# Kernel tuning notes

Hardware: AMD Instinct MI355X
Metric: run time of the kernel (lower is better)

The kernel has to match this reference:

```python
import jax, jax.numpy as jnp
import numpy as np

B, C, PC, P = 64, 32, 128, 2048
N = B * C * PC          # 262144 graph nodes
E = 2097152             # ~8 edges per node


def _gcn(x, src, dst, n, W, b):
    # PyG GCNConv: add self loops, sym-normalized mean aggregation of x@W
    xw = x @ W
    sl = jnp.arange(n, dtype=src.dtype)
    s = jnp.concatenate([src, sl]); d = jnp.concatenate([dst, sl])
    deg = jax.ops.segment_sum(jnp.ones(d.shape, xw.dtype), d, num_segments=n)
    dinv = jax.lax.rsqrt(deg)  # deg >= 1 thanks to self loops
    norm = dinv[s] * dinv[d]
    return jax.ops.segment_sum(xw[s] * norm[:, None], d, num_segments=n) + b


def _gat(x, src, dst, n, W, a_src, a_dst, b):
    # PyG GATConv (heads=1): self loops, edge softmax over incoming edges
    xw = x @ W
    sl = jnp.arange(n, dtype=src.dtype)
    s = jnp.concatenate([src, sl]); d = jnp.concatenate([dst, sl])
    e = jax.nn.leaky_relu((xw @ a_src)[s] + (xw @ a_dst)[d], 0.2)
    m = jax.ops.segment_max(jax.lax.stop_gradient(e), d, num_segments=n)
    ex = jnp.exp(e - m[d])
    denom = jax.ops.segment_sum(ex, d, num_segments=n)
    alpha = ex / denom[d]
    return jax.ops.segment_sum(xw[s] * alpha[:, None], d, num_segments=n) + b


def _cross_edges(num_cross, batch_size):
    # faithful to get_c_adjacency: every ordered pair (i!=j) appears twice per graph
    ii, jj = np.meshgrid(np.arange(num_cross), np.arange(num_cross), indexing='ij')
    m = ii != jj
    s, d = ii[m], jj[m]
    s2 = np.concatenate([s, d]); d2 = np.concatenate([d, s])
    off = (np.arange(batch_size) * num_cross)[:, None]
    src = (s2[None] + off).reshape(-1)
    dst = (d2[None] + off).reshape(-1)
    return jnp.asarray(src, jnp.int32), jnp.asarray(dst, jnp.int32)


def _conv1d(x, W, b):
    y = jax.lax.conv_general_dilated(x, W, (2,), ((1, 1),), dimension_numbers=('NCH', 'OIH', 'NCH'))
    return y + b[None, :, None]


def _bn_eval(x, gamma, beta):
    # BatchNorm1d in eval mode with default running stats (mean 0, var 1)
    scale = gamma / np.float32(np.sqrt(1.0 + 1e-5))
    return x * scale[None, :, None] + beta[None, :, None]


def setup_inputs() -> dict:
    key = jax.random.key(0)
    ks = jax.random.split(key, 32)
    rn = lambda k, sh, s=0.1: (jax.random.normal(k, sh, jnp.float32) * s)
    return {
        'x': jax.random.normal(ks[0], (N, 19), jnp.float32),
        'edge_index': jax.random.randint(ks[1], (2, E), 0, N, jnp.int32),
        'points': jax.random.normal(ks[2], (B, 3, P), jnp.float32),
        'W1': rn(ks[3], (19, 32)), 'b1': rn(ks[4], (32,)),
        'W2': rn(ks[5], (32, 64)), 'b2': rn(ks[6], (64,)),
        'W3': rn(ks[7], (64, 64)), 'b3': rn(ks[8], (64,)),
        'Wg1': rn(ks[9], (64, 64)), 'asrc1': rn(ks[10], (64,)), 'adst1': rn(ks[11], (64,)), 'bg1': rn(ks[12], (64,)),
        'Wg2': rn(ks[13], (64, 64)), 'asrc2': rn(ks[14], (64,)), 'adst2': rn(ks[15], (64,)), 'bg2': rn(ks[16], (64,)),
        'c1W': rn(ks[17], (32, 3, 3)), 'c1b': rn(ks[18], (32,)),
        'g1': 1.0 + rn(ks[19], (32,)), 'be1': rn(ks[20], (32,)),
        'c2W': rn(ks[21], (64, 32, 3)), 'c2b': rn(ks[22], (64,)),
        'g2': 1.0 + rn(ks[23], (64,)), 'be2': rn(ks[24], (64,)),
        'c3W': rn(ks[25], (64, 64, 3)), 'c3b': rn(ks[26], (64,)),
        'Wl2': rn(ks[27], (64, 64)), 'bl2': rn(ks[28], (64,)),
        'Wl3': rn(ks[29], (64, 1)), 'bl3': rn(ks[30], (1,)),
        'batch_size': B, 'num_cross': C, 'num_pieces': PC,
    }


def reference(x, edge_index, points, W1, b1, W2, b2, W3, b3,
              Wg1, asrc1, adst1, bg1, Wg2, asrc2, adst2, bg2,
              c1W, c1b, g1, be1, c2W, c2b, g2, be2, c3W, c3b,
              Wl2, bl2, Wl3, bl3, batch_size, num_cross, num_pieces):
    src, dst = edge_index[0], edge_index[1]
    n = x.shape[0]
    h = jax.nn.relu(_gcn(x, src, dst, n, W1, b1))  # dropout is a no-op in eval
    h = jax.nn.leaky_relu(_gcn(h, src, dst, n, W2, b2), 0.01)
    h = jax.nn.leaky_relu(_gcn(h, src, dst, n, W3, b3), 0.01)
    h = _gat(h, src, dst, n, Wg1, asrc1, adst1, bg1)
    h = h.reshape(batch_size, num_cross, num_pieces, -1).mean(-2)  # [B, C, 64]
    s2, d2 = _cross_edges(num_cross, batch_size)
    h = _gat(h.reshape(batch_size * num_cross, 64), s2, d2, batch_size * num_cross, Wg2, asrc2, adst2, bg2)
    h = h.reshape(batch_size, num_cross, 64).mean(1)  # [B, 64]
    p = _bn_eval(jax.nn.leaky_relu(_conv1d(points, c1W, c1b), 0.01), g1, be1)
    p = _bn_eval(jax.nn.leaky_relu(_conv1d(p, c2W, c2b), 0.01), g2, be2)
    p = jax.nn.leaky_relu(_conv1d(p, c3W, c3b), 0.01).mean(-1)  # AdaptiveAvgPool1d(1).squeeze -> [B, 64]
    h = h + p
    h = jax.nn.leaky_relu(h @ Wl2 + bl2, 0.01)
    return jax.nn.sigmoid(h @ Wl3 + bl3)  # [B, 1]
```

## Files before the change

kernel.cpp:

```cpp
#include <hip/hip_runtime.h>
#include <cstdint>
#include <cstddef>

#define NN 262144
#define EE 2097152
#define BB 64
#define CCROSS 32
#define PCC 128
#define PP 2048
#define NBUCK 256
#define BCAP 12288

typedef _Float16 f16;
typedef __attribute__((ext_vector_type(4))) _Float16 f16x4;
typedef __attribute__((ext_vector_type(8))) _Float16 f16x8;
typedef __attribute__((ext_vector_type(4))) float f32x4;

static __device__ __forceinline__ float lrelu(float x, float s) { return x > 0.f ? x : s * x; }

__global__ __launch_bounds__(256) void bucket_a_k(const int* __restrict__ src, const int* __restrict__ dst,
                                                  unsigned* __restrict__ buckets, int* __restrict__ gcnt) {
    __shared__ int hist[NBUCK];
    __shared__ int base[NBUCK];
    __shared__ unsigned short rankbuf[8192];
    const int tid = threadIdx.x;
    const int e0 = blockIdx.x * 8192;
    hist[tid] = 0;
    __syncthreads();
    for (int i = tid; i < 8192; i += 256) {
        int d = dst[e0 + i];
        rankbuf[i] = (unsigned short)atomicAdd(&hist[d >> 10], 1);
    }
    __syncthreads();
    base[tid] = tid * BCAP + atomicAdd(&gcnt[tid], hist[tid]);
    __syncthreads();
    for (int i = tid; i < 8192; i += 256) {
        int s = src[e0 + i];
        int d = dst[e0 + i];
        int b = d >> 10;
        buckets[base[b] + rankbuf[i]] = ((unsigned)s << 10) | (unsigned)(d & 1023);
    }
}

__global__ void bucket_scan_k(const int* __restrict__ gcnt, int* __restrict__ bbase, int* __restrict__ rp) {
    __shared__ int tmp[256];
    int tid = threadIdx.x;
    int v = gcnt[tid];
    tmp[tid] = v;
    __syncthreads();
    for (int off = 1; off < 256; off <<= 1) {
        int t = (tid >= off) ? tmp[tid - off] : 0;
        __syncthreads();
        tmp[tid] += t;
        __syncthreads();
    }
    bbase[tid] = tmp[tid] - v;
    if (tid == 0) rp[NN] = EE;
}

__global__ __launch_bounds__(256) void bucket_b_k(const unsigned* __restrict__ buckets, const int* __restrict__ gcnt,
                                                  const int* __restrict__ bbase, int* __restrict__ rp,
                                                  float* __restrict__ dinv, int* __restrict__ col) {
    __shared__ int cnt[1024];
    __shared__ int scan[1024];
    __shared__ int wsum[256];
    const int b = blockIdx.x;
    const int tid = threadIdx.x;
    int n = gcnt[b];
    if (n > BCAP) n = BCAP;
    const unsigned* eb = buckets + (size_t)b * BCAP;
    const int gb = bbase[b];
    for (int i = tid; i < 1024; i += 256) cnt[i] = 0;
    __syncthreads();
    for (int i = tid; i < n; i += 256) atomicAdd(&cnt[eb[i] & 1023], 1);
    __syncthreads();
    int b4 = tid * 4;
    int c0 = cnt[b4], c1 = cnt[b4 + 1], c2 = cnt[b4 + 2], c3 = cnt[b4 + 3];
    int tsum = c0 + c1 + c2 + c3;
    wsum[tid] = tsum;
    __syncthreads();
    for (int off = 1; off < 256; off <<= 1) {
        int t = (tid >= off) ? wsum[tid - off] : 0;
        __syncthreads();
        wsum[tid] += t;
        __syncthreads();
    }
    int excl = wsum[tid] - tsum;
    scan[b4] = excl;
    scan[b4 + 1] = excl + c0;
    scan[b4 + 2] = excl + c0 + c1;
    scan[b4 + 3] = excl + c0 + c1 + c2;
    int vbase = b * 1024 + b4;
    rp[vbase + 0] = gb + scan[b4 + 0];
    rp[vbase + 1] = gb + scan[b4 + 1];
    rp[vbase + 2] = gb + scan[b4 + 2];
    rp[vbase + 3] = gb + scan[b4 + 3];
    dinv[vbase + 0] = rsqrtf((float)(c0 + 1));
    dinv[vbase + 1] = rsqrtf((float)(c1 + 1));
    dinv[vbase + 2] = rsqrtf((float)(c2 + 1));
    dinv[vbase + 3] = rsqrtf((float)(c3 + 1));
    __syncthreads();
    for (int i = tid; i < 1024; i += 256) cnt[i] = 0;
    __syncthreads();
    for (int i = tid; i < n; i += 256) {
        unsigned p = eb[i];
        int dl = p & 1023;
        int r = atomicAdd(&cnt[dl], 1);
        col[gb + scan[dl] + r] = (int)(p >> 10);
    }
}

__global__ void zprep_k(const float* __restrict__ x, const float* __restrict__ dinv, f16* __restrict__ z) {
    int v = blockIdx.x * 256 + threadIdx.x;
    if (v >= NN) return;
    float dv = dinv[v];
    const float* xr = x + (size_t)v * 19;
    float vv[20];
#pragma unroll
    for (int k = 0; k < 19; k++) vv[k] = dv * xr[k];
    vv[19] = 0.f;
    f16x4* zr = (f16x4*)(z + (size_t)v * 32);
#pragma unroll
    for (int c = 0; c < 5; c++) {
        f16x4 t = {(f16)vv[4 * c], (f16)vv[4 * c + 1], (f16)vv[4 * c + 2], (f16)vv[4 * c + 3]};
        zr[c] = t;
    }
    f16x4 zz = {(f16)0.f, (f16)0.f, (f16)0.f, (f16)0.f};
#pragma unroll
    for (int c = 5; c < 8; c++) zr[c] = zz;
}

#define ZSTR1 36
template <int KINR, int KOUT, int ACT>
__global__ __launch_bounds__(256) void fused_agg_gemm_k(const f16* __restrict__ z, const int* __restrict__ rp,
                                                        const int* __restrict__ col, const float* __restrict__ Wg,
                                                        const float* __restrict__ dinv, const float* __restrict__ bias,
                                                        f16* __restrict__ zout) {
    constexpr int NO = KOUT / 4;
    __shared__ float Wl[32 * KOUT];
    __shared__ float zrow[64 * ZSTR1];
    const int tid = threadIdx.x;
    for (int i = tid; i < 32 * KOUT; i += 256) Wl[i] = (i < KINR * KOUT) ? Wg[i] : 0.f;

    const int r = tid >> 2;
    const int idx = tid & 3;
    const int v = blockIdx.x * 64 + r;
    const f16x8* z8 = (const f16x8*)z;
    f16x8 a = z8[(size_t)v * 4 + idx];
    float acc8[8];
#pragma unroll
    for (int j = 0; j < 8; j++) acc8[j] = (float)a[j];
    int st = rp[v], e = rp[v + 1];
    int i = st;
    for (; i + 4 <= e; i += 4) {
        int u0 = col[i], u1 = col[i + 1], u2 = col[i + 2], u3 = col[i + 3];
        f16x8 a0 = z8[(size_t)u0 * 4 + idx];
        f16x8 a1 = z8[(size_t)u1 * 4 + idx];
        f16x8 a2 = z8[(size_t)u2 * 4 + idx];
        f16x8 a3 = z8[(size_t)u3 * 4 + idx];
#pragma unroll
        for (int j = 0; j < 8; j++)
            acc8[j] += ((float)a0[j] + (float)a1[j]) + ((float)a2[j] + (float)a3[j]);
    }
    for (; i < e; i++) {
        f16x8 aa = z8[(size_t)col[i] * 4 + idx];
#pragma unroll
        for (int j = 0; j < 8; j++) acc8[j] += (float)aa[j];
    }
    float4 s0, s1;
    s0.x = acc8[0]; s0.y = acc8[1]; s0.z = acc8[2]; s0.w = acc8[3];
    s1.x = acc8[4]; s1.y = acc8[5]; s1.z = acc8[6]; s1.w = acc8[7];
    *(float4*)&zrow[r * ZSTR1 + idx * 8] = s0;
    *(float4*)&zrow[r * ZSTR1 + idx * 8 + 4] = s1;
    __syncthreads();

    float acc[NO];
#pragma unroll
    for (int j = 0; j < NO; j++) acc[j] = 0.f;
#pragma unroll 4
    for (int k = 0; k < 32; k++) {
        float zv = zrow[r * ZSTR1 + k];
        const float* wr = Wl + k * KOUT + NO * idx;
#pragma unroll
        for (int j = 0; j < NO; j++) acc[j] = fmaf(zv, wr[j], acc[j]);
    }
    float dv = dinv[v];
    f16 hv[NO];
#pragma unroll
    for (int j = 0; j < NO; j++) {
        float o = dv * acc[j] + bias[NO * idx + j];
        o = (ACT == 0) ? fmaxf(o, 0.f) : lrelu(o, 0.01f);
        hv[j] = (f16)(o * dv);
    }
    if constexpr (NO == 8) {
        f16x8 h = {hv[0], hv[1], hv[2], hv[3], hv[4], hv[5], hv[6], hv[7]};
        *(f16x8*)(zout + (size_t)v * KOUT + NO * idx) = h;
    } else {
        f16x8 h0 = {hv[0], hv[1], hv[2], hv[3], hv[4], hv[5], hv[6], hv[7]};
        f16x8 h1 = {hv[8], hv[9], hv[10], hv[11], hv[12], hv[13], hv[14], hv[15]};
        f16x8* yo = (f16x8*)(zout + (size_t)v * KOUT + NO * idx);
        yo[0] = h0; yo[1] = h1;
    }
}

__global__ __launch_bounds__(256) void agg_h16_k(const f16* __restrict__ y, const int* __restrict__ rp,
                                                 const int* __restrict__ col, f16* __restrict__ out) {
    int gid = blockIdx.x * 256 + threadIdx.x;
    int v = gid >> 3;
    int idx = gid & 7;
    const f16x8* y8 = (const f16x8*)y;
    f16x8 a = y8[(size_t)v * 8 + idx];
    float acc[8];
#pragma unroll
    for (int j = 0; j < 8; j++) acc[j] = (float)a[j];
    int s = rp[v], e = rp[v + 1];
    int i = s;
    for (; i + 4 <= e; i += 4) {
        int u0 = col[i], u1 = col[i + 1], u2 = col[i + 2], u3 = col[i + 3];
        f16x8 a0 = y8[(size_t)u0 * 8 + idx];
        f16x8 a1 = y8[(size_t)u1 * 8 + idx];
        f16x8 a2 = y8[(size_t)u2 * 8 + idx];
        f16x8 a3 = y8[(size_t)u3 * 8 + idx];
#pragma unroll
        for (int j = 0; j < 8; j++)
            acc[j] += ((float)a0[j] + (float)a1[j]) + ((float)a2[j] + (float)a3[j]);
    }
    for (; i < e; i++) {
        f16x8 aa = y8[(size_t)col[i] * 8 + idx];
#pragma unroll
        for (int j = 0; j < 8; j++) acc[j] += (float)aa[j];
    }
    f16x8 r;
#pragma unroll
    for (int j = 0; j < 8; j++) r[j] = (f16)acc[j];
    ((f16x8*)out)[(size_t)v * 8 + idx] = r;
}

__global__ void pack_w_k(const float* __restrict__ W, f16* __restrict__ out) {
    int o = blockIdx.x * 256 + threadIdx.x;
    if (o >= 4096) return;
    int frag = o >> 9;
    int kt = frag >> 2;
    int c = frag & 3;
    int idx = o & 511;
    int l = idx >> 3;
    int j = idx & 7;
    int k = kt * 32 + ((l >> 4) << 3) + j;
    int n = 16 * c + (l & 15);
    out[o] = (f16)W[k * 64 + n];
}

#define HSTR 72
__global__ __launch_bounds__(256) void gemm3_gat_k(const f16* __restrict__ aggz, const f16* __restrict__ w3p,
                                                   const float* __restrict__ dinv, const float* __restrict__ b3,
                                                   const f16* __restrict__ wgp, const float* __restrict__ av,
                                                   const float* __restrict__ ad, f16* __restrict__ xw,
                                                   float* __restrict__ es, float* __restrict__ ed) {
    __shared__ f16 zin[64 * HSTR];
    __shared__ f16 hh[64 * HSTR];
    const int tid = threadIdx.x;
    const int v0 = blockIdx.x * 64;
    {
        int row = tid >> 2;
        int kb = (tid & 3) * 16;
        const f16x8* zp = (const f16x8*)(aggz + (size_t)(v0 + row) * 64 + kb);
        f16x8 z0 = zp[0], z1 = zp[1];
        *(f16x8*)&zin[row * HSTR + kb] = z0;
        *(f16x8*)&zin[row * HSTR + kb + 8] = z1;
    }
    __syncthreads();

    const int w = tid >> 6;
    const int l = tid & 63;
    const int m = l & 15;
    const int q = l >> 4;
    const int r0 = 16 * w;

    f32x4 acc0 = {0.f, 0.f, 0.f, 0.f}, acc1 = acc0, acc2 = acc0, acc3 = acc0;
#pragma unroll
    for (int kt = 0; kt < 2; kt++) {
        f16x8 afrag = *(const f16x8*)&zin[(r0 + m) * HSTR + kt * 32 + q * 8];
        f16x8 b0 = *(const f16x8*)&w3p[((kt * 4 + 0) << 9) + l * 8];
        f16x8 b1 = *(const f16x8*)&w3p[((kt * 4 + 1) << 9) + l * 8];
        f16x8 b2 = *(const f16x8*)&w3p[((kt * 4 + 2) << 9) + l * 8];
        f16x8 b3f = *(const f16x8*)&w3p[((kt * 4 + 3) << 9) + l * 8];
        acc0 = __builtin_amdgcn_mfma_f32_16x16x32_f16(afrag, b0, acc0, 0, 0, 0);
        acc1 = __builtin_amdgcn_mfma_f32_16x16x32_f16(afrag, b1, acc1, 0, 0, 0);
        acc2 = __builtin_amdgcn_mfma_f32_16x16x32_f16(afrag, b2, acc2, 0, 0, 0);
        acc3 = __builtin_amdgcn_mfma_f32_16x16x32_f16(afrag, b3f, acc3, 0, 0, 0);
    }
    {
        float dv0 = dinv[v0 + r0 + q * 4 + 0];
        float dv1 = dinv[v0 + r0 + q * 4 + 1];
        float dv2 = dinv[v0 + r0 + q * 4 + 2];
        float dv3 = dinv[v0 + r0 + q * 4 + 3];
#pragma unroll
        for (int c = 0; c < 4; c++) {
            const f32x4* ac = (c == 0) ? &acc0 : (c == 1) ? &acc1 : (c == 2) ? &acc2 : &acc3;
            float bb = b3[16 * c + m];
            hh[(r0 + q * 4 + 0) * HSTR + 16 * c + m] = (f16)lrelu(dv0 * (*ac)[0] + bb, 0.01f);
            hh[(r0 + q * 4 + 1) * HSTR + 16 * c + m] = (f16)lrelu(dv1 * (*ac)[1] + bb, 0.01f);
            hh[(r0 + q * 4 + 2) * HSTR + 16 * c + m] = (f16)lrelu(dv2 * (*ac)[2] + bb, 0.01f);
            hh[(r0 + q * 4 + 3) * HSTR + 16 * c + m] = (f16)lrelu(dv3 * (*ac)[3] + bb, 0.01f);
        }
    }
    __syncthreads();

    acc0 = (f32x4){0.f, 0.f, 0.f, 0.f}; acc1 = acc0; acc2 = acc0; acc3 = acc0;
#pragma unroll
    for (int kt = 0; kt < 2; kt++) {
        f16x8 afrag = *(const f16x8*)&hh[(r0 + m) * HSTR + kt * 32 + q * 8];
        f16x8 b0 = *(const f16x8*)&wgp[((kt * 4 + 0) << 9) + l * 8];
        f16x8 b1 = *(const f16x8*)&wgp[((kt * 4 + 1) << 9) + l * 8];
        f16x8 b2 = *(const f16x8*)&wgp[((kt * 4 + 2) << 9) + l * 8];
        f16x8 b3f = *(const f16x8*)&wgp[((kt * 4 + 3) << 9) + l * 8];
        acc0 = __builtin_amdgcn_mfma_f32_16x16x32_f16(afrag, b0, acc0, 0, 0, 0);
        acc1 = __builtin_amdgcn_mfma_f32_16x16x32_f16(afrag, b1, acc1, 0, 0, 0);
        acc2 = __builtin_amdgcn_mfma_f32_16x16x32_f16(afrag, b2, acc2, 0, 0, 0);
        acc3 = __builtin_amdgcn_mfma_f32_16x16x32_f16(afrag, b3f, acc3, 0, 0, 0);
    }
    {
        float e1[4] = {0.f, 0.f, 0.f, 0.f}, e2[4] = {0.f, 0.f, 0.f, 0.f};
#pragma unroll
        for (int c = 0; c < 4; c++) {
            const f32x4* ac = (c == 0) ? &acc0 : (c == 1) ? &acc1 : (c == 2) ? &acc2 : &acc3;
            float a1 = av[16 * c + m];
            float d1 = ad[16 * c + m];
#pragma unroll
            for (int reg = 0; reg < 4; reg++) {
                float g = (*ac)[reg];
                e1[reg] = fmaf(g, a1, e1[reg]);
                e2[reg] = fmaf(g, d1, e2[reg]);
                xw[(size_t)(v0 + r0 + q * 4 + reg) * 64 + 16 * c + m] = (f16)g;
            }
        }
#pragma unroll
        for (int reg = 0; reg < 4; reg++) {
            e1[reg] += __shfl_xor(e1[reg], 1); e1[reg] += __shfl_xor(e1[reg], 2);
            e1[reg] += __shfl_xor(e1[reg], 4); e1[reg] += __shfl_xor(e1[reg], 8);
            e2[reg] += __shfl_xor(e2[reg], 1); e2[reg] += __shfl_xor(e2[reg], 2);
            e2[reg] += __shfl_xor(e2[reg], 4); e2[reg] += __shfl_xor(e2[reg], 8);
        }
        if (m == 0) {
#pragma unroll
            for (int reg = 0; reg < 4; reg++) {
                es[v0 + r0 + q * 4 + reg] = e1[reg];
                ed[v0 + r0 + q * 4 + reg] = e2[reg];
            }
        }
    }
}

__global__ void gat_w_k(const float* __restrict__ es, const float* __restrict__ ed,
                        const int* __restrict__ rp, const int* __restrict__ col,
                        f16* __restrict__ ew, float* __restrict__ wself, float* __restrict__ invden) {
    int v = blockIdx.x * 256 + threadIdx.x;
    if (v >= NN) return;
    float edv = ed[v];
    float eself = lrelu(es[v] + edv, 0.2f);
    float m = eself;
    int s = rp[v], e = rp[v + 1];
    int i = s;
    float lg[32];
    for (; i + 4 <= e; i += 4) {
        int u0 = col[i], u1 = col[i + 1], u2 = col[i + 2], u3 = col[i + 3];
        float t0 = lrelu(es[u0] + edv, 0.2f);
        float t1 = lrelu(es[u1] + edv, 0.2f);
        float t2 = lrelu(es[u2] + edv, 0.2f);
        float t3 = lrelu(es[u3] + edv, 0.2f);
        int k = i - s;
        if (k + 3 < 32) { lg[k] = t0; lg[k + 1] = t1; lg[k + 2] = t2; lg[k + 3] = t3; }
        m = fmaxf(m, fmaxf(fmaxf(t0, t1), fmaxf(t2, t3)));
    }
    for (; i < e; i++) {
        float t = lrelu(es[col[i]] + edv, 0.2f);
        int k = i - s;
        if (k < 32) lg[k] = t;
        m = fmaxf(m, t);
    }
    float wsl = __expf(eself - m);
    float den = wsl;
    for (i = s; i < e; i++) {
        int k = i - s;
        float t = (k < 32) ? lg[k] : lrelu(es[col[i]] + edv, 0.2f);
        float w = __expf(t - m);
        ew[i] = (f16)w;
        den += w;
    }
    wself[v] = wsl;
    invden[v] = 1.f / den;
}

__global__ __launch_bounds__(256) void gat_agg_h_k(const f16* __restrict__ y, const int* __restrict__ rp,
                                                   const int* __restrict__ col, const f16* __restrict__ ew,
                                                   const float* __restrict__ wself, const float* __restrict__ invden,
                                                   const float* __restrict__ bias, float* __restrict__ out) {
    int gid = blockIdx.x * 256 + threadIdx.x;
    int v = gid >> 3;
    int idx = gid & 7;
    const f16x8* y8 = (const f16x8*)y;
    float ws = wself[v];
    f16x8 self = y8[(size_t)v * 8 + idx];
    float acc[8];
#pragma unroll
    for (int j = 0; j < 8; j++) acc[j] = ws * (float)self[j];
    int s = rp[v], e = rp[v + 1];
    int i = s;
    for (; i + 4 <= e; i += 4) {
        int u0 = col[i], u1 = col[i + 1], u2 = col[i + 2], u3 = col[i + 3];
        float w0 = (float)ew[i], w1 = (float)ew[i + 1], w2 = (float)ew[i + 2], w3 = (float)ew[i + 3];
        f16x8 a0 = y8[(size_t)u0 * 8 + idx];
        f16x8 a1 = y8[(size_t)u1 * 8 + idx];
        f16x8 a2 = y8[(size_t)u2 * 8 + idx];
        f16x8 a3 = y8[(size_t)u3 * 8 + idx];
#pragma unroll
        for (int j = 0; j < 8; j++)
            acc[j] = fmaf(w0, (float)a0[j], fmaf(w1, (float)a1[j], fmaf(w2, (float)a2[j], fmaf(w3, (float)a3[j], acc[j]))));
    }
    for (; i < e; i++) {
        float w = (float)ew[i];
        f16x8 aa = y8[(size_t)col[i] * 8 + idx];
#pragma unroll
        for (int j = 0; j < 8; j++) acc[j] = fmaf(w, (float)aa[j], acc[j]);
    }
    float inv = invden[v];
    const float4* b4 = (const float4*)(bias + 8 * idx);
    float4 bb0 = b4[0], bb1 = b4[1];
    float4 o0, o1;
    o0.x = acc[0] * inv + bb0.x; o0.y = acc[1] * inv + bb0.y;
    o0.z = acc[2] * inv + bb0.z; o0.w = acc[3] * inv + bb0.w;
    o1.x = acc[4] * inv + bb1.x; o1.y = acc[5] * inv + bb1.y;
    o1.z = acc[6] * inv + bb1.z; o1.w = acc[7] * inv + bb1.w;
    float4* op = (float4*)(out + (size_t)v * 64 + 8 * idx);
    op[0] = o0; op[1] = o1;
}

__global__ void pool_pieces_k(const float* __restrict__ in, float* __restrict__ out) {
    int gid = blockIdx.x * 256 + threadIdx.x;
    if (gid >= BB * CCROSS * 64) return;
    int f = gid & 63, g = gid >> 6;
    const float* p = in + (size_t)g * PCC * 64 + f;
    float s = 0.f;
#pragma unroll 8
    for (int i = 0; i < PCC; i++) s += p[(size_t)i * 64];
    out[gid] = s * (1.f / 128.f);
}

__global__ void pool_cross_k(const float* __restrict__ in, float* __restrict__ out) {
    int gid = blockIdx.x * 64 + threadIdx.x;
    if (gid >= BB * 64) return;
    int f = gid & 63, b = gid >> 6;
    const float* p = in + (size_t)b * CCROSS * 64 + f;
    float s = 0.f;
#pragma unroll
    for (int i = 0; i < CCROSS; i++) s += p[(size_t)i * 64];
    out[gid] = s * (1.f / 32.f);
}

template <int KIN, int KOUT>
__global__ void gat_gemm_k(const float* __restrict__ x, const float* __restrict__ W,
                           float* __restrict__ y, const float* __restrict__ av, const float* __restrict__ ad,
                           float* __restrict__ es, float* __restrict__ ed, int n) {
    int v = blockIdx.x * 256 + threadIdx.x;
    if (v >= n) return;
    const float* xr = x + (size_t)v * KIN;
    float acc[KOUT];
#pragma unroll
    for (int j = 0; j < KOUT; j++) acc[j] = 0.f;
#pragma unroll 2
    for (int k = 0; k < KIN; k++) {
        float xv = xr[k];
#pragma unroll
        for (int j = 0; j < KOUT; j++) acc[j] = fmaf(xv, W[k * KOUT + j], acc[j]);
    }
    float e1 = 0.f, e2 = 0.f;
    float4* y4 = (float4*)(y + (size_t)v * KOUT);
#pragma unroll
    for (int j4 = 0; j4 < KOUT / 4; j4++) {
        float4 t;
        t.x = acc[4 * j4 + 0]; t.y = acc[4 * j4 + 1]; t.z = acc[4 * j4 + 2]; t.w = acc[4 * j4 + 3];
        y4[j4] = t;
        e1 = fmaf(t.x, av[4 * j4 + 0], e1); e1 = fmaf(t.y, av[4 * j4 + 1], e1);
        e1 = fmaf(t.z, av[4 * j4 + 2], e1); e1 = fmaf(t.w, av[4 * j4 + 3], e1);
        e2 = fmaf(t.x, ad[4 * j4 + 0], e2); e2 = fmaf(t.y, ad[4 * j4 + 1], e2);
        e2 = fmaf(t.z, ad[4 * j4 + 2], e2); e2 = fmaf(t.w, ad[4 * j4 + 3], e2);
    }
    es[v] = e1; ed[v] = e2;
}

__global__ void cross_att_k(const float* __restrict__ xw, const float* __restrict__ es,
                            const float* __restrict__ ed, const float* __restrict__ bg,
                            float* __restrict__ out) {
    int gid = blockIdx.x * 256 + threadIdx.x;
    if (gid >= BB * CCROSS * 64) return;
    int f = gid & 63;
    int d = (gid >> 6) & 31;
    int g = gid >> 11;
    int base = g * CCROSS;
    float edd = ed[base + d];
    float m = -1e30f;
#pragma unroll
    for (int s = 0; s < CCROSS; s++) {
        float e = lrelu(es[base + s] + edd, 0.2f);
        m = fmaxf(m, e);
    }
    float den = 0.f, acc = 0.f;
#pragma unroll
    for (int s = 0; s < CCROSS; s++) {
        float e = lrelu(es[base + s] + edd, 0.2f);
        float w = __expf(e - m) * ((s == d) ? 1.f : 2.f);
        den += w;
        acc = fmaf(w, xw[(size_t)(base + s) * 64 + f], acc);
    }
    out[gid] = acc / den + bg[f];
}

#define S0_STR 264
#define S1_STR 132
#define S2_STR 66
#define S0_OFF 0
#define S1_OFF (3 * S0_STR)
#define S2_OFF (S1_OFF + 32 * S1_STR)
#define SMEM_FLOATS (S2_OFF + 64 * S2_STR)

__global__ __launch_bounds__(256) void conv_fused_k(
        const float* __restrict__ pts, const float* __restrict__ c1W, const float* __restrict__ c1b,
        const float* __restrict__ g1, const float* __restrict__ be1,
        const float* __restrict__ c2W, const float* __restrict__ c2b,
        const float* __restrict__ g2, const float* __restrict__ be2,
        const float* __restrict__ c3W, const float* __restrict__ c3b,
        float* __restrict__ partials) {
    __shared__ float smem[SMEM_FLOATS];
    float* s0 = smem + S0_OFF;
    float* s1 = smem + S1_OFF;
    float* s2 = smem + S2_OFF;
    float* s3 = smem;

    const int b = blockIdx.x >> 3;
    const int q = blockIdx.x & 7;
    const int tid = threadIdx.x;
    const float bnscale = 0.99999500003749968f;

    const int lo0 = 256 * q - 7;
    for (int t = tid; t < 3 * 263; t += 256) {
        int c = t / 263, j = t - c * 263;
        int p = lo0 + j;
        s0[c * S0_STR + j] = (p >= 0 && p < PP) ? pts[((size_t)b * 3 + c) * PP + p] : 0.f;
    }
    __syncthreads();

    const int lo1 = 128 * q - 3;
    for (int t = tid; t < 32 * 131; t += 256) {
        int ch = t / 131, j = t - ch * 131;
        int p1 = lo1 + j;
        float v = 0.f;
        if (p1 >= 0 && p1 < 1024) {
            float acc = c1b[ch];
            const float* w = c1W + ch * 9;
            const float* x0 = s0 + 2 * j;
#pragma unroll
            for (int ci = 0; ci < 3; ci++) {
                acc = fmaf(x0[ci * S0_STR + 0], w[ci * 3 + 0], acc);
                acc = fmaf(x0[ci * S0_STR + 1], w[ci * 3 + 1], acc);
                acc = fmaf(x0[ci * S0_STR + 2], w[ci * 3 + 2], acc);
            }
            acc = lrelu(acc, 0.01f);
            v = fmaf(acc, g1[ch] * bnscale, be1[ch]);
        }
        s1[ch * S1_STR + j] = v;
    }
    __syncthreads();

    const int lo2 = 64 * q - 1;
    for (int t = tid; t < 64 * 65; t += 256) {
        int ch = t / 65, j = t - ch * 65;
        int p2 = lo2 + j;
        float v = 0.f;
        if (p2 >= 0 && p2 < 512) {
            float acc = c2b[ch];
            const float* w = c2W + ch * 96;
            const float* x1 = s1 + 2 * j;
#pragma unroll
            for (int ci = 0; ci < 32; ci++) {
                acc = fmaf(x1[ci * S1_STR + 0], w[ci * 3 + 0], acc);
                acc = fmaf(x1[ci * S1_STR + 1], w[ci * 3 + 1], acc);
                acc = fmaf(x1[ci * S1_STR + 2], w[ci * 3 + 2], acc);
            }
            acc = lrelu(acc, 0.01f);
            v = fmaf(acc, g2[ch] * bnscale, be2[ch]);
        }
        s2[ch * S2_STR + j] = v;
    }
    __syncthreads();

    for (int t = tid; t < 64 * 32; t += 256) {
        int o = t >> 5, j = t & 31;
        float acc = c3b[o];
        const float* w = c3W + o * 192;
        const float* x2 = s2 + 2 * j;
#pragma unroll 16
        for (int ci = 0; ci < 64; ci++) {
            acc = fmaf(x2[ci * S2_STR + 0], w[ci * 3 + 0], acc);
            acc = fmaf(x2[ci * S2_STR + 1], w[ci * 3 + 1], acc);
            acc = fmaf(x2[ci * S2_STR + 2], w[ci * 3 + 2], acc);
        }
        s3[t] = lrelu(acc, 0.01f);
    }
    __syncthreads();

    if (tid < 64) {
        float s = 0.f;
#pragma unroll
        for (int j = 0; j < 32; j++) s += s3[tid * 32 + j];
        partials[((size_t)b * 8 + q) * 64 + tid] = s;
    }
}

__global__ void head_k(const float* __restrict__ hG, const float* __restrict__ partials,
                       const float* __restrict__ Wl2, const float* __restrict__ bl2,
                       const float* __restrict__ Wl3, const float* __restrict__ bl3,
                       float* __restrict__ out) {
    int b = blockIdx.x;
    int f = threadIdx.x;
    __shared__ float sh[64];
    float p = 0.f;
#pragma unroll
    for (int q = 0; q < 8; q++) p += partials[((size_t)b * 8 + q) * 64 + f];
    float h = hG[b * 64 + f] + p * (1.f / 256.f);
    sh[f] = h;
    __syncthreads();
    float acc = bl2[f];
#pragma unroll
    for (int k = 0; k < 64; k++) acc = fmaf(sh[k], Wl2[k * 64 + f], acc);
    acc = lrelu(acc, 0.01f);
    float pr = acc * Wl3[f];
#pragma unroll
    for (int off = 32; off > 0; off >>= 1) pr += __shfl_down(pr, off, 64);
    if (f == 0) out[b] = 1.f / (1.f + __expf(-(pr + bl3[0])));
}

extern "C" void kernel_launch(void* const* d_in, const int* in_sizes, int n_in,
                              void* d_out, int out_size, void* d_ws, size_t ws_size,
                              hipStream_t stream) {
    const float* x = (const float*)d_in[0];
    const int* ei = (const int*)d_in[1];
    const float* points = (const float*)d_in[2];
    const float* W1 = (const float*)d_in[3];
    const float* b1 = (const float*)d_in[4];
    const float* W2 = (const float*)d_in[5];
    const float* b2 = (const float*)d_in[6];
    const float* W3 = (const float*)d_in[7];
    const float* b3 = (const float*)d_in[8];
    const float* Wg1 = (const float*)d_in[9];
    const float* asrc1 = (const float*)d_in[10];
    const float* adst1 = (const float*)d_in[11];
    const float* bg1 = (const float*)d_in[12];
    const float* Wg2 = (const float*)d_in[13];
    const float* asrc2 = (const float*)d_in[14];
    const float* adst2 = (const float*)d_in[15];
    const float* bg2 = (const float*)d_in[16];
    const float* c1W = (const float*)d_in[17];
    const float* c1b = (const float*)d_in[18];
    const float* g1 = (const float*)d_in[19];
    const float* be1 = (const float*)d_in[20];
    const float* c2W = (const float*)d_in[21];
    const float* c2b = (const float*)d_in[22];
    const float* g2 = (const float*)d_in[23];
    const float* be2 = (const float*)d_in[24];
    const float* c3W = (const float*)d_in[25];
    const float* c3b = (const float*)d_in[26];
    const float* Wl2 = (const float*)d_in[27];
    const float* bl2 = (const float*)d_in[28];
    const float* Wl3 = (const float*)d_in[29];
    const float* bl3 = (const float*)d_in[30];

    const int* src = ei;
    const int* dst = ei + EE;

    char* w = (char*)d_ws;
    size_t off = 0;
    auto A = [&](size_t bytes) -> void* {
        void* p = w + off;
        off = (off + bytes + 255) & ~(size_t)255;
        return p;
    };
    int* colb = (int*)A((size_t)EE * 4);
    int* rp = (int*)A((size_t)(NN + 1) * 4);
    int* gcnt = (int*)A(NBUCK * 4);
    int* bbase = (int*)A(NBUCK * 4);
    float* dinv = (float*)A((size_t)NN * 4);
    float* bufA = (float*)A((size_t)NN * 64 * 4);
    f16* bufH1 = (f16*)A((size_t)NN * 64 * 2);
    f16* bufH2 = (f16*)A((size_t)NN * 64 * 2);
    f16* ew = (f16*)A((size_t)EE * 2);
    float* wself = (float*)A((size_t)NN * 4);
    float* invden = (float*)A((size_t)NN * 4);
    float* es = (float*)A((size_t)NN * 4);
    float* edv = (float*)A((size_t)NN * 4);
    f16* w3p = (f16*)A(4096 * 2);
    f16* wgp = (f16*)A(4096 * 2);
    float* pooled = (float*)A((size_t)BB * CCROSS * 64 * 4);
    float* xw2 = (float*)A((size_t)BB * CCROSS * 64 * 4);
    float* es2 = (float*)A((size_t)BB * CCROSS * 4);
    float* ed2 = (float*)A((size_t)BB * CCROSS * 4);
    float* crosso = (float*)A((size_t)BB * CCROSS * 64 * 4);
    float* hG = (float*)A((size_t)BB * 64 * 4);
    float* partials = (float*)A((size_t)BB * 8 * 64 * 4);

    unsigned* buckets = (unsigned*)bufA;
    f16* aggH = (f16*)bufA;

    hipMemsetAsync(gcnt, 0, NBUCK * 4, stream);
    bucket_a_k<<<EE / 8192, 256, 0, stream>>>(src, dst, buckets, gcnt);
    bucket_scan_k<<<1, 256, 0, stream>>>(gcnt, bbase, rp);
    bucket_b_k<<<NBUCK, 256, 0, stream>>>(buckets, gcnt, bbase, rp, dinv, colb);

    conv_fused_k<<<BB * 8, 256, 0, stream>>>(points, c1W, c1b, g1, be1, c2W, c2b, g2, be2, c3W, c3b, partials);
    pack_w_k<<<16, 256, 0, stream>>>(W3, w3p);
    pack_w_k<<<16, 256, 0, stream>>>(Wg1, wgp);

    zprep_k<<<NN / 256, 256, 0, stream>>>(x, dinv, bufH1);
    fused_agg_gemm_k<19, 32, 0><<<NN / 64, 256, 0, stream>>>(bufH1, rp, colb, W1, dinv, b1, bufH2);
    fused_agg_gemm_k<32, 64, 1><<<NN / 64, 256, 0, stream>>>(bufH2, rp, colb, W2, dinv, b2, bufH1);
    agg_h16_k<<<(NN * 8) / 256, 256, 0, stream>>>(bufH1, rp, colb, aggH);
    gemm3_gat_k<<<NN / 64, 256, 0, stream>>>(aggH, w3p, dinv, b3, wgp, asrc1, adst1,
                                             bufH2, es, edv);

    gat_w_k<<<NN / 256, 256, 0, stream>>>(es, edv, rp, colb, ew, wself, invden);
    gat_agg_h_k<<<(NN * 8) / 256, 256, 0, stream>>>(bufH2, rp, colb, ew, wself, invden, bg1, bufA);

    pool_pieces_k<<<(BB * CCROSS * 64) / 256, 256, 0, stream>>>(bufA, pooled);
    gat_gemm_k<64, 64><<<(BB * CCROSS) / 256, 256, 0, stream>>>(pooled, Wg2, xw2, asrc2, adst2, es2, ed2, BB * CCROSS);
    cross_att_k<<<(BB * CCROSS * 64) / 256, 256, 0, stream>>>(xw2, es2, ed2, bg2, crosso);
    pool_cross_k<<<BB, 64, 0, stream>>>(crosso, hG);

    head_k<<<BB, 64, 0, stream>>>(hG, partials, Wl2, bl2, Wl3, bl3, (float*)d_out);
}
```

Measured before the change: 533.9 us.

## Rewrite conv branch with fp16 channel-last smem and register-resident packed weights

Conv layers 2 and 3 of the point branch now store activations in shared memory channel-last as fp16 and compute with packed f16 dot2 instructions. Each thread holds one output channel's weights in registers, prepacked by two new small kernels. The final reduction uses per-thread partial sums in place of a strided shared-memory sum. This cuts scalar FMA count and global weight reads in the conv kernel, at the cost of fp16 rounding of intermediate activations, two extra launches, and higher register pressure.

Measured after the change: 510.4 us. 1.05x faster.

```diff
diff --git a/kernel.cpp b/kernel.cpp
--- a/kernel.cpp
+++ b/kernel.cpp
@@ -12,11 +12,24 @@
 #define BCAP 12288
 
 typedef _Float16 f16;
+typedef __attribute__((ext_vector_type(2))) _Float16 f16x2;
 typedef __attribute__((ext_vector_type(4))) _Float16 f16x4;
 typedef __attribute__((ext_vector_type(8))) _Float16 f16x8;
 typedef __attribute__((ext_vector_type(4))) float f32x4;
 
 static __device__ __forceinline__ float lrelu(float x, float s) { return x > 0.f ? x : s * x; }
+
+#if __has_builtin(__builtin_amdgcn_fdot2)
+static __device__ __forceinline__ float dot2f(unsigned x, unsigned w, float c) {
+    return __builtin_amdgcn_fdot2(__builtin_bit_cast(f16x2, x), __builtin_bit_cast(f16x2, w), c, false);
+}
+#else
+static __device__ __forceinline__ float dot2f(unsigned x, unsigned w, float c) {
+    f16x2 a = __builtin_bit_cast(f16x2, x);
+    f16x2 b = __builtin_bit_cast(f16x2, w);
+    return fmaf((float)a[0], (float)b[0], fmaf((float)a[1], (float)b[1], c));
+}
+#endif
 
 __global__ __launch_bounds__(256) void bucket_a_k(const int* __restrict__ src, const int* __restrict__ dst,
                                                   unsigned* __restrict__ buckets, int* __restrict__ gcnt) {
@@ -248,6 +261,22 @@
     int k = kt * 32 + ((l >> 4) << 3) + j;
     int n = 16 * c + (l & 15);
     out[o] = (f16)W[k * 64 + n];
+}
+
+__global__ void pack_c2_k(const float* __restrict__ W, f16* __restrict__ out) {
+    int o = blockIdx.x * 256 + threadIdx.x;
+    if (o >= 64 * 96) return;
+    int ch = o / 96, r = o - ch * 96;
+    int k = r >> 5, ci = r & 31;
+    out[o] = (f16)W[ch * 96 + ci * 3 + k];
+}
+
+__global__ void pack_c3_k(const float* __restrict__ W, f16* __restrict__ out) {
+    int o = blockIdx.x * 256 + threadIdx.x;
+    if (o >= 64 * 192) return;
+    int ch = o / 192, r = o - ch * 192;
+    int k = r >> 6, ci = r & 63;
+    out[o] = (f16)W[ch * 192 + ci * 3 + k];
 }
 
 #define HSTR 72
@@ -515,26 +544,17 @@
     out[gid] = acc / den + bg[f];
 }
 
-#define S0_STR 264
-#define S1_STR 132
-#define S2_STR 66
-#define S0_OFF 0
-#define S1_OFF (3 * S0_STR)
-#define S2_OFF (S1_OFF + 32 * S1_STR)
-#define SMEM_FLOATS (S2_OFF + 64 * S2_STR)
-
 __global__ __launch_bounds__(256) void conv_fused_k(
         const float* __restrict__ pts, const float* __restrict__ c1W, const float* __restrict__ c1b,
         const float* __restrict__ g1, const float* __restrict__ be1,
-        const float* __restrict__ c2W, const float* __restrict__ c2b,
+        const f16* __restrict__ w2p, const float* __restrict__ c2b,
         const float* __restrict__ g2, const float* __restrict__ be2,
-        const float* __restrict__ c3W, const float* __restrict__ c3b,
+        const f16* __restrict__ w3pc, const float* __restrict__ c3b,
         float* __restrict__ partials) {
-    __shared__ float smem[SMEM_FLOATS];
-    float* s0 = smem + S0_OFF;
-    float* s1 = smem + S1_OFF;
-    float* s2 = smem + S2_OFF;
-    float* s3 = smem;
+    __shared__ __align__(16) float s0[3 * 264];
+    __shared__ __align__(16) f16 s1T[132 * 32];
+    __shared__ __align__(16) f16 s2T[66 * 64];
+    __shared__ float sred[256];
 
     const int b = blockIdx.x >> 3;
     const int q = blockIdx.x & 7;
@@ -545,73 +565,127 @@
     for (int t = tid; t < 3 * 263; t += 256) {
         int c = t / 263, j = t - c * 263;
         int p = lo0 + j;
-        s0[c * S0_STR + j] = (p >= 0 && p < PP) ? pts[((size_t)b * 3 + c) * PP + p] : 0.f;
-    }
-    __syncthreads();
-
-    const int lo1 = 128 * q - 3;
-    for (int t = tid; t < 32 * 131; t += 256) {
-        int ch = t / 131, j = t - ch * 131;
-        int p1 = lo1 + j;
-        float v = 0.f;
-        if (p1 >= 0 && p1 < 1024) {
-            float acc = c1b[ch];
-            const float* w = c1W + ch * 9;
-            const float* x0 = s0 + 2 * j;
-#pragma unroll
-            for (int ci = 0; ci < 3; ci++) {
-                acc = fmaf(x0[ci * S0_STR + 0], w[ci * 3 + 0], acc);
-                acc = fmaf(x0[ci * S0_STR + 1], w[ci * 3 + 1], acc);
-                acc = fmaf(x0[ci * S0_STR + 2], w[ci * 3 + 2], acc);
+        s0[c * 264 + j] = (p >= 0 && p < PP) ? pts[((size_t)b * 3 + c) * PP + p] : 0.f;
+    }
+    __syncthreads();
+
+    {
+        const int ch = tid & 31;
+        const int j0 = tid >> 5;
+        float wv[9];
+        const float* wg = c1W + ch * 9;
+#pragma unroll
+        for (int t = 0; t < 9; t++) wv[t] = wg[t];
+        const float bs = c1b[ch];
+        const float gs = g1[ch] * bnscale;
+        const float bt = be1[ch];
+        const int lo1 = 128 * q - 3;
+        for (int j = j0; j < 131; j += 8) {
+            int p1 = lo1 + j;
+            float v = 0.f;
+            if (p1 >= 0 && p1 < 1024) {
+                const float* x0 = s0 + 2 * j;
+                float a0 = bs, a1 = 0.f, a2 = 0.f;
+#pragma unroll
+                for (int c = 0; c < 3; c++) {
+                    float2 x01 = *(const float2*)(x0 + c * 264);
+                    float x2v = x0[c * 264 + 2];
+                    a0 = fmaf(x01.x, wv[c * 3 + 0], a0);
+                    a1 = fmaf(x01.y, wv[c * 3 + 1], a1);
+                    a2 = fmaf(x2v, wv[c * 3 + 2], a2);
+                }
+                float acc = a0 + a1 + a2;
+                acc = lrelu(acc, 0.01f);
+                v = fmaf(acc, gs, bt);
             }
-            acc = lrelu(acc, 0.01f);
-            v = fmaf(acc, g1[ch] * bnscale, be1[ch]);
+            s1T[j * 32 + ch] = (f16)v;
         }
-        s1[ch * S1_STR + j] = v;
-    }
-    __syncthreads();
-
-    const int lo2 = 64 * q - 1;
-    for (int t = tid; t < 64 * 65; t += 256) {
-        int ch = t / 65, j = t - ch * 65;
-        int p2 = lo2 + j;
-        float v = 0.f;
-        if (p2 >= 0 && p2 < 512) {
-            float acc = c2b[ch];
-            const float* w = c2W + ch * 96;
-            const float* x1 = s1 + 2 * j;
-#pragma unroll
-            for (int ci = 0; ci < 32; ci++) {
-                acc = fmaf(x1[ci * S1_STR + 0], w[ci * 3 + 0], acc);
-                acc = fmaf(x1[ci * S1_STR + 1], w[ci * 3 + 1], acc);
-                acc = fmaf(x1[ci * S1_STR + 2], w[ci * 3 + 2], acc);
+    }
+    __syncthreads();
+
+    {
+        const int ch = tid & 63;
+        const int jg = tid >> 6;
+        unsigned wr[48];
+        const uint4* wp = (const uint4*)(w2p + (size_t)ch * 96);
+#pragma unroll
+        for (int t = 0; t < 12; t++) {
+            uint4 u = wp[t];
+            wr[4 * t + 0] = u.x; wr[4 * t + 1] = u.y; wr[4 * t + 2] = u.z; wr[4 * t + 3] = u.w;
+        }
+        const float bs = c2b[ch];
+        const float gs = g2[ch] * bnscale;
+        const float bt = be2[ch];
+        const int lo2v = 64 * q - 1;
+        for (int j = jg; j < 65; j += 4) {
+            float ak[3] = {bs, 0.f, 0.f};
+#pragma unroll
+            for (int k = 0; k < 3; k++) {
+                const uint4* xp = (const uint4*)(s1T + (2 * j + k) * 32);
+                uint4 x0 = xp[0], x1 = xp[1], x2 = xp[2], x3 = xp[3];
+                float a = ak[k];
+                a = dot2f(x0.x, wr[k * 16 + 0], a);
+                a = dot2f(x0.y, wr[k * 16 + 1], a);
+                a = dot2f(x0.z, wr[k * 16 + 2], a);
+                a = dot2f(x0.w, wr[k * 16 + 3], a);
+                a = dot2f(x1.x, wr[k * 16 + 4], a);
+                a = dot2f(x1.y, wr[k * 16 + 5], a);
+                a = dot2f(x1.z, wr[k * 16 + 6], a);
+                a = dot2f(x1.w, wr[k * 16 + 7], a);
+                a = dot2f(x2.x, wr[k * 16 + 8], a);
+                a = dot2f(x2.y, wr[k * 16 + 9], a);
+                a = dot2f(x2.z, wr[k * 16 + 10], a);
+                a = dot2f(x2.w, wr[k * 16 + 11], a);
+                a = dot2f(x3.x, wr[k * 16 + 12], a);
+                a = dot2f(x3.y, wr[k * 16 + 13], a);
+                a = dot2f(x3.z, wr[k * 16 + 14], a);
+                a = dot2f(x3.w, wr[k * 16 + 15], a);
+                ak[k] = a;
             }
-            acc = lrelu(acc, 0.01f);
-            v = fmaf(acc, g2[ch] * bnscale, be2[ch]);
+            float acc = ak[0] + ak[1] + ak[2];
+            int p2 = lo2v + j;
+            float v = 0.f;
+            if (p2 >= 0 && p2 < 512) v = fmaf(lrelu(acc, 0.01f), gs, bt);
+            s2T[j * 64 + ch] = (f16)v;
         }
-        s2[ch * S2_STR + j] = v;
-    }
-    __syncthreads();
-
-    for (int t = tid; t < 64 * 32; t += 256) {
-        int o = t >> 5, j = t & 31;
-        float acc = c3b[o];
-        const float* w = c3W + o * 192;
-        const float* x2 = s2 + 2 * j;
-#pragma unroll 16
-        for (int ci = 0; ci < 64; ci++) {
-            acc = fmaf(x2[ci * S2_STR + 0], w[ci * 3 + 0], acc);
-            acc = fmaf(x2[ci * S2_STR + 1], w[ci * 3 + 1], acc);
-            acc = fmaf(x2[ci * S2_STR + 2], w[ci * 3 + 2], acc);
+    }
+    __syncthreads();
+
+    {
+        const int ch = tid & 63;
+        const int jg = tid >> 6;
+        unsigned wr[96];
+        const uint4* wp = (const uint4*)(w3pc + (size_t)ch * 192);
+#pragma unroll
+        for (int t = 0; t < 24; t++) {
+            uint4 u = wp[t];
+            wr[4 * t + 0] = u.x; wr[4 * t + 1] = u.y; wr[4 * t + 2] = u.z; wr[4 * t + 3] = u.w;
         }
-        s3[t] = lrelu(acc, 0.01f);
-    }
-    __syncthreads();
-
+        const float bs = c3b[ch];
+        float psum = 0.f;
+        for (int j = jg; j < 32; j += 4) {
+            float ak[3] = {bs, 0.f, 0.f};
+#pragma unroll
+            for (int k = 0; k < 3; k++) {
+                const uint4* xp = (const uint4*)(s2T + (2 * j + k) * 64);
+                float a = ak[k];
+#pragma unroll
+                for (int t = 0; t < 8; t++) {
+                    uint4 xv = xp[t];
+                    a = dot2f(xv.x, wr[k * 32 + 4 * t + 0], a);
+                    a = dot2f(xv.y, wr[k * 32 + 4 * t + 1], a);
+                    a = dot2f(xv.z, wr[k * 32 + 4 * t + 2], a);
+                    a = dot2f(xv.w, wr[k * 32 + 4 * t + 3], a);
+                }
+                ak[k] = a;
+            }
+            psum += lrelu(ak[0] + ak[1] + ak[2], 0.01f);
+        }
+        sred[tid] = psum;
+    }
+    __syncthreads();
     if (tid < 64) {
-        float s = 0.f;
-#pragma unroll
-        for (int j = 0; j < 32; j++) s += s3[tid * 32 + j];
+        float s = sred[tid] + sred[tid + 64] + sred[tid + 128] + sred[tid + 192];
         partials[((size_t)b * 8 + q) * 64 + tid] = s;
     }
 }
@@ -699,6 +773,8 @@
     float* edv = (float*)A((size_t)NN * 4);
     f16* w3p = (f16*)A(4096 * 2);
     f16* wgp = (f16*)A(4096 * 2);
+    f16* wc2p = (f16*)A(64 * 96 * 2);
+    f16* wc3p = (f16*)A(64 * 192 * 2);
     float* pooled = (float*)A((size_t)BB * CCROSS * 64 * 4);
     float* xw2 = (float*)A((size_t)BB * CCROSS * 64 * 4);
     float* es2 = (float*)A((size_t)BB * CCROSS * 4);
@@ -715,7 +791,9 @@
     bucket_scan_k<<<1, 256, 0, stream>>>(gcnt, bbase, rp);
     bucket_b_k<<<NBUCK, 256, 0, stream>>>(buckets, gcnt, bbase, rp, dinv, colb);
 
-    conv_fused_k<<<BB * 8, 256, 0, stream>>>(points, c1W, c1b, g1, be1, c2W, c2b, g2, be2, c3W, c3b, partials);
+    pack_c2_k<<<24, 256, 0, stream>>>(c2W, wc2p);
+    pack_c3_k<<<48, 256, 0, stream>>>(c3W, wc3p);
+    conv_fused_k<<<BB * 8, 256, 0, stream>>>(points, c1W, c1b, g1, be1, wc2p, c2b, g2, be2, wc3p, c3b, partials);
     pack_w_k<<<16, 256, 0, stream>>>(W3, w3p);
     pack_w_k<<<16, 256, 0, stream>>>(Wg1, wgp);
 
```
